# Optimization experiments

Hardware: AMD Instinct MI355X
Metric: run time of the kernel (lower is better)

## Reference

```python
import jax, jax.numpy as jnp
import numpy as np

LN_EPS = 1e-5

def setup_inputs() -> dict:
    key = jax.random.key(0)
    ks = jax.random.split(key, 8)
    B, d, var_dim, hidden = 1024, 32, 64, 256
    in_dim = d * var_dim
    causal_vars = jax.random.normal(ks[0], (B, d, var_dim), dtype=jnp.float32)
    adj_soft = jax.random.uniform(ks[1], (d, d), dtype=jnp.float32)
    # Per-variable MLP params (stacked along leading d axis), torch-default-like init scale
    s1 = 1.0 / np.sqrt(in_dim)
    s2 = 1.0 / np.sqrt(hidden)
    W1 = jax.random.uniform(ks[2], (d, in_dim, hidden), minval=-s1, maxval=s1, dtype=jnp.float32)
    b1 = jax.random.uniform(ks[3], (d, hidden), minval=-s1, maxval=s1, dtype=jnp.float32)
    W2 = jax.random.uniform(ks[4], (d, hidden, var_dim), minval=-s2, maxval=s2, dtype=jnp.float32)
    b2 = jax.random.uniform(ks[5], (d, var_dim), minval=-s2, maxval=s2, dtype=jnp.float32)
    gamma = jnp.ones((d, var_dim), dtype=jnp.float32)
    beta = jnp.zeros((d, var_dim), dtype=jnp.float32)
    return {"causal_vars": causal_vars, "adj_soft": adj_soft, "W1": W1, "b1": b1,
            "W2": W2, "b2": b2, "gamma": gamma, "beta": beta}

def reference(causal_vars, adj_soft, W1, b1, W2, b2, gamma, beta):
    B, d, var_dim = causal_vars.shape
    # masked parent input for equation i: adj_soft[i, j] * causal_vars[b, j, :]
    # shape (B, d_eq, d_parent, var_dim) -> flatten parents: (B, d, d*var_dim)
    x = adj_soft[None, :, :, None] * causal_vars[:, None, :, :]
    x = x.reshape(B, d, d * var_dim)
    # grouped 2-layer MLP, distinct weights per variable i
    h = jnp.einsum('bik,ikh->bih', x, W1) + b1[None]
    h = jax.nn.gelu(h, approximate=False)
    y = jnp.einsum('bih,ihv->biv', h, W2) + b2[None]
    # LayerNorm over var_dim with per-variable affine params
    mu = jnp.mean(y, axis=-1, keepdims=True)
    var = jnp.var(y, axis=-1, keepdims=True)
    y = (y - mu) * jax.lax.rsqrt(var + LN_EPS)
    return y * gamma[None] + beta[None]  # (B, d, var_dim)
```

## Files before the change

### kernel.cpp

```cpp
#include <hip/hip_runtime.h>
#include <hip/hip_bf16.h>

typedef __bf16 bf16_t;
typedef __bf16 bf16x8 __attribute__((ext_vector_type(8)));
typedef float f32x4 __attribute__((ext_vector_type(4)));

#define NB 1024
#define ND 32
#define VD 64
#define NH 256
#define NK 2048

#define OFF_A    0
#define OFF_W1T  (4u*1024u*1024u)
#define OFF_W2T  (36u*1024u*1024u)

#define GLD16(gsrc, ldst) \
  __builtin_amdgcn_global_load_lds((const __attribute__((address_space(1))) void*)(gsrc), \
                                   (__attribute__((address_space(3))) void*)(ldst), 16, 0, 0)

__global__ __launch_bounds__(256) void prep_kernel(
    const float* __restrict__ cv, const float* __restrict__ adj,
    const float* __restrict__ W1, const float* __restrict__ W2,
    bf16_t* __restrict__ A, bf16_t* __restrict__ W1T, bf16_t* __restrict__ W2T)
{
  __shared__ float Ls[64 * 67];
  int bx = blockIdx.x;
  int tid = threadIdx.x;
  if (bx < 4096) {
    int i = bx >> 7;
    int rem = bx & 127;
    int k0 = (rem >> 2) * 64;
    int h0 = (rem & 3) * 64;
    float a = adj[i * 32 + (k0 >> 6)];
    int rrow = tid >> 4, c4 = (tid & 15) * 4;
#pragma unroll
    for (int p = 0; p < 4; ++p) {
      int row = p * 16 + rrow;
      const float* src = W1 + ((size_t)(i * 2048 + k0 + row)) * 256 + h0 + c4;
      float4 v = *(const float4*)src;
#pragma unroll
      for (int j = 0; j < 4; ++j) Ls[row * 67 + c4 + j] = a * ((const float*)&v)[j];
    }
    __syncthreads();
#pragma unroll
    for (int p = 0; p < 2; ++p) {
      int u = p * 256 + tid;
      int h = u >> 3, c8 = u & 7;
      bf16x8 o;
#pragma unroll
      for (int j = 0; j < 8; ++j) o[j] = (bf16_t)Ls[(c8 * 8 + j) * 67 + h];
      *(bf16x8*)(W1T + ((size_t)(i * 256 + h0 + h)) * 2048 + k0 + c8 * 8) = o;
    }
  } else if (bx < 5120) {
    int t = (bx - 4096) * 256 + tid;
    const float4* s = (const float4*)cv + (size_t)t * 2;
    float4 v0 = s[0], v1 = s[1];
    bf16x8 o;
    o[0] = (bf16_t)v0.x; o[1] = (bf16_t)v0.y; o[2] = (bf16_t)v0.z; o[3] = (bf16_t)v0.w;
    o[4] = (bf16_t)v1.x; o[5] = (bf16_t)v1.y; o[6] = (bf16_t)v1.z; o[7] = (bf16_t)v1.w;
    *(bf16x8*)(A + (size_t)t * 8) = o;
  } else {
    int t = (bx - 5120) * 256 + tid;
    int i = t >> 11;
    int rem = t & 2047;
    int h8 = rem >> 6;
    int v = rem & 63;
    const float* src = W2 + ((size_t)(i * 256 + h8 * 8)) * 64 + v;
    bf16x8 o;
#pragma unroll
    for (int r = 0; r < 8; ++r) o[r] = (bf16_t)src[(size_t)r * 64];
    *(bf16x8*)(W2T + ((size_t)(i * 64 + v)) * 256 + h8 * 8) = o;
  }
}

__global__ __launch_bounds__(512, 4) void sem_main_kernel(
    const bf16_t* __restrict__ A, const bf16_t* __restrict__ W1T,
    const bf16_t* __restrict__ W2T,
    const float* __restrict__ b1, const float* __restrict__ b2,
    const float* __restrict__ gamma, const float* __restrict__ beta,
    float* __restrict__ out)
{
  __shared__ char smem[61440];

  int p = blockIdx.x;
  int L = (p & 7) * 64 + (p >> 3);
  int i = L >> 4;
  int brow = (L & 15) * 64;

  int tid = threadIdx.x;
  int lane = tid & 63;
  int wid = tid >> 6;
  int wr = wid >> 2;
  int wc = wid & 3;
  int lhi = lane >> 4;
  int llo = lane & 15;

  const bf16_t* W1Ti = W1T + (size_t)i * 256 * 2048;

  int arow = tid >> 2, ac = tid & 3;
  int sc0 = ac ^ ((arow >> 1) & 3);
  const bf16_t* aSrc  = A + (size_t)(brow + arow) * 2048 + sc0 * 8;
  const bf16_t* bSrc0 = W1Ti + (size_t)arow * 2048 + sc0 * 8;
  const bf16_t* bSrc1 = W1Ti + (size_t)(128 + arow) * 2048 + sc0 * 8;
  int ldsW = wid * 1024;

  auto stage = [&](int b, int kt) {
    char* base = smem + b * 20480;
    if (wid < 4) GLD16(aSrc + (size_t)kt * 32, base + ldsW);
    GLD16(bSrc0 + (size_t)kt * 32, base + 4096 + ldsW);
    GLD16(bSrc1 + (size_t)kt * 32, base + 12288 + ldsW);
  };

  int aOff[2], bOff[4];
#pragma unroll
  for (int m = 0; m < 2; ++m) {
    int row = wr * 32 + m * 16 + llo;
    aOff[m] = row * 64 + ((lhi ^ ((row >> 1) & 3)) * 16);
  }
#pragma unroll
  for (int n = 0; n < 4; ++n) {
    int row = wc * 64 + n * 16 + llo;
    bOff[n] = 4096 + row * 64 + ((lhi ^ ((row >> 1) & 3)) * 16);
  }

  f32x4 acc[2][4];
#pragma unroll
  for (int m = 0; m < 2; ++m)
#pragma unroll
    for (int n = 0; n < 4; ++n) acc[m][n] = (f32x4){0.f, 0.f, 0.f, 0.f};

  auto compute = [&](int b) {
    const char* base = smem + b * 20480;
    bf16x8 af[2], bfr[4];
#pragma unroll
    for (int m = 0; m < 2; ++m) af[m] = *(const bf16x8*)(base + aOff[m]);
#pragma unroll
    for (int n = 0; n < 4; ++n) bfr[n] = *(const bf16x8*)(base + bOff[n]);
    __builtin_amdgcn_s_setprio(1);
#pragma unroll
    for (int m = 0; m < 2; ++m)
#pragma unroll
      for (int n = 0; n < 4; ++n)
        acc[m][n] = __builtin_amdgcn_mfma_f32_16x16x32_bf16(af[m], bfr[n], acc[m][n], 0, 0, 0);
    __builtin_amdgcn_s_setprio(0);
  };

#define WAIT_OWN_TILE() do { \
    if (wid < 4) asm volatile("s_waitcnt vmcnt(3) lgkmcnt(0)" ::: "memory"); \
    else         asm volatile("s_waitcnt vmcnt(2) lgkmcnt(0)" ::: "memory"); \
  } while (0)

  asm volatile("" ::: "memory");
  stage(0, 0); stage(1, 1);
  int bc = 0, bs = 2;
  for (int t = 0; t < 62; ++t) {
    WAIT_OWN_TILE();
    __builtin_amdgcn_s_barrier();
    asm volatile("" ::: "memory");
    stage(bs, t + 2);
    compute(bc);
    bc = (bc == 2) ? 0 : bc + 1;
    bs = (bs == 2) ? 0 : bs + 1;
  }
  WAIT_OWN_TILE();
  __builtin_amdgcn_s_barrier();
  asm volatile("" ::: "memory");
  compute(2);
  asm volatile("s_waitcnt vmcnt(0) lgkmcnt(0)" ::: "memory");
  __builtin_amdgcn_s_barrier();
  asm volatile("" ::: "memory");
  compute(0);
  __syncthreads();

  bf16_t* Hs = (bf16_t*)smem;
  float bias[4];
#pragma unroll
  for (int n = 0; n < 4; ++n) bias[n] = b1[i * 256 + wc * 64 + n * 16 + llo];
#pragma unroll
  for (int m = 0; m < 2; ++m) {
#pragma unroll
    for (int n = 0; n < 4; ++n) {
      int col = wc * 64 + n * 16 + llo;
#pragma unroll
      for (int r = 0; r < 4; ++r) {
        int row = wr * 32 + m * 16 + lhi * 4 + r;
        float x = acc[m][n][r] + bias[n];
        float gl = 0.5f * x * (1.0f + erff(x * 0.70710678118654752f));
        Hs[row * 264 + col] = (bf16_t)gl;
      }
    }
  }
  __syncthreads();

  if (wid < 4) {
    f32x4 acc2[4];
#pragma unroll
    for (int n = 0; n < 4; ++n) acc2[n] = (f32x4){0.f, 0.f, 0.f, 0.f};
    const bf16_t* W2Ti = W2T + (size_t)i * 64 * 256;
#pragma unroll
    for (int kk = 0; kk < 8; ++kk) {
      int k = kk * 32 + lhi * 8;
      bf16x8 af = *(const bf16x8*)(Hs + (wid * 16 + llo) * 264 + k);
#pragma unroll
      for (int n = 0; n < 4; ++n) {
        bf16x8 bfr = *(const bf16x8*)(W2Ti + (size_t)(n * 16 + llo) * 256 + k);
        acc2[n] = __builtin_amdgcn_mfma_f32_16x16x32_bf16(af, bfr, acc2[n], 0, 0, 0);
      }
    }
    float b2v[4], gam[4], bet[4];
#pragma unroll
    for (int n = 0; n < 4; ++n) {
      int v = n * 16 + llo;
      b2v[n] = b2[i * 64 + v];
      gam[n] = gamma[i * 64 + v];
      bet[n] = beta[i * 64 + v];
    }
#pragma unroll
    for (int r = 0; r < 4; ++r) {
      float yv[4], s = 0.f, sq = 0.f;
#pragma unroll
      for (int n = 0; n < 4; ++n) {
        yv[n] = acc2[n][r] + b2v[n];
        s += yv[n];
        sq += yv[n] * yv[n];
      }
#pragma unroll
      for (int off = 1; off < 16; off <<= 1) {
        s += __shfl_xor(s, off, 64);
        sq += __shfl_xor(sq, off, 64);
      }
      float mu = s * (1.0f / 64.0f);
      float var = sq * (1.0f / 64.0f) - mu * mu;
      float rstd = rsqrtf(var + 1e-5f);
      int row = brow + wid * 16 + lhi * 4 + r;
      float* op = out + ((size_t)row * 32 + i) * 64;
#pragma unroll
      for (int n = 0; n < 4; ++n)
        op[n * 16 + llo] = (yv[n] - mu) * rstd * gam[n] + bet[n];
    }
  }
}

extern "C" void kernel_launch(void* const* d_in, const int* in_sizes, int n_in,
                              void* d_out, int out_size, void* d_ws, size_t ws_size,
                              hipStream_t stream) {
  const float* cv    = (const float*)d_in[0];
  const float* adj   = (const float*)d_in[1];
  const float* W1    = (const float*)d_in[2];
  const float* b1    = (const float*)d_in[3];
  const float* W2    = (const float*)d_in[4];
  const float* b2    = (const float*)d_in[5];
  const float* gamma = (const float*)d_in[6];
  const float* beta  = (const float*)d_in[7];
  float* out = (float*)d_out;

  bf16_t* Abf  = (bf16_t*)((char*)d_ws + OFF_A);
  bf16_t* W1T  = (bf16_t*)((char*)d_ws + OFF_W1T);
  bf16_t* W2T  = (bf16_t*)((char*)d_ws + OFF_W2T);

  prep_kernel<<<5376, 256, 0, stream>>>(cv, adj, W1, W2, Abf, W1T, W2T);
  sem_main_kernel<<<512, 512, 0, stream>>>(Abf, W1T, W2T, b1, b2, gamma, beta, out);
}
```

Measured before the change: 78.50 us.

## Replace LDS triple-buffered GEMM1 pipeline with direct global-to-register MFMA loads

Drops the global_load_lds triple-buffered staging, the swizzled LDS layout and the barriers in the first GEMM. Each wave now loads its MFMA fragments straight from global memory into registers in a 4x-unrolled loop, and the LDS allocation shrinks to what the hidden-activation buffer needs. This removes barrier and LDS traffic and may raise occupancy. In exchange, A and W1T tiles are no longer shared across waves, so each wave re-reads them from global or L2, and latency hiding now depends on the compiler's scheduling of the unrolled loads.

```diff
diff --git a/kernel.cpp b/kernel.cpp
--- a/kernel.cpp
+++ b/kernel.cpp
@@ -15,9 +15,7 @@
 #define OFF_W1T  (4u*1024u*1024u)
 #define OFF_W2T  (36u*1024u*1024u)
 
-#define GLD16(gsrc, ldst) \
-  __builtin_amdgcn_global_load_lds((const __attribute__((address_space(1))) void*)(gsrc), \
-                                   (__attribute__((address_space(3))) void*)(ldst), 16, 0, 0)
+#define MFMA16(AF, BF, ACC) __builtin_amdgcn_mfma_f32_16x16x32_bf16(AF, BF, ACC, 0, 0, 0)
 
 __global__ __launch_bounds__(256) void prep_kernel(
     const float* __restrict__ cv, const float* __restrict__ adj,
@@ -81,7 +79,7 @@
     const float* __restrict__ gamma, const float* __restrict__ beta,
     float* __restrict__ out)
 {
-  __shared__ char smem[61440];
+  __shared__ char smem[33792];
 
   int p = blockIdx.x;
   int L = (p & 7) * 64 + (p >> 3);
@@ -98,31 +96,8 @@
 
   const bf16_t* W1Ti = W1T + (size_t)i * 256 * 2048;
 
-  int arow = tid >> 2, ac = tid & 3;
-  int sc0 = ac ^ ((arow >> 1) & 3);
-  const bf16_t* aSrc  = A + (size_t)(brow + arow) * 2048 + sc0 * 8;
-  const bf16_t* bSrc0 = W1Ti + (size_t)arow * 2048 + sc0 * 8;
-  const bf16_t* bSrc1 = W1Ti + (size_t)(128 + arow) * 2048 + sc0 * 8;
-  int ldsW = wid * 1024;
-
-  auto stage = [&](int b, int kt) {
-    char* base = smem + b * 20480;
-    if (wid < 4) GLD16(aSrc + (size_t)kt * 32, base + ldsW);
-    GLD16(bSrc0 + (size_t)kt * 32, base + 4096 + ldsW);
-    GLD16(bSrc1 + (size_t)kt * 32, base + 12288 + ldsW);
-  };
-
-  int aOff[2], bOff[4];
-#pragma unroll
-  for (int m = 0; m < 2; ++m) {
-    int row = wr * 32 + m * 16 + llo;
-    aOff[m] = row * 64 + ((lhi ^ ((row >> 1) & 3)) * 16);
-  }
-#pragma unroll
-  for (int n = 0; n < 4; ++n) {
-    int row = wc * 64 + n * 16 + llo;
-    bOff[n] = 4096 + row * 64 + ((lhi ^ ((row >> 1) & 3)) * 16);
-  }
+  const bf16_t* aP = A + (size_t)(brow + wr * 32 + llo) * 2048 + lhi * 8;
+  const bf16_t* bP = W1Ti + (size_t)(wc * 64 + llo) * 2048 + lhi * 8;
 
   f32x4 acc[2][4];
 #pragma unroll
@@ -130,48 +105,25 @@
 #pragma unroll
     for (int n = 0; n < 4; ++n) acc[m][n] = (f32x4){0.f, 0.f, 0.f, 0.f};
 
-  auto compute = [&](int b) {
-    const char* base = smem + b * 20480;
-    bf16x8 af[2], bfr[4];
-#pragma unroll
-    for (int m = 0; m < 2; ++m) af[m] = *(const bf16x8*)(base + aOff[m]);
-#pragma unroll
-    for (int n = 0; n < 4; ++n) bfr[n] = *(const bf16x8*)(base + bOff[n]);
-    __builtin_amdgcn_s_setprio(1);
-#pragma unroll
-    for (int m = 0; m < 2; ++m)
-#pragma unroll
-      for (int n = 0; n < 4; ++n)
-        acc[m][n] = __builtin_amdgcn_mfma_f32_16x16x32_bf16(af[m], bfr[n], acc[m][n], 0, 0, 0);
-    __builtin_amdgcn_s_setprio(0);
-  };
-
-#define WAIT_OWN_TILE() do { \
-    if (wid < 4) asm volatile("s_waitcnt vmcnt(3) lgkmcnt(0)" ::: "memory"); \
-    else         asm volatile("s_waitcnt vmcnt(2) lgkmcnt(0)" ::: "memory"); \
-  } while (0)
-
-  asm volatile("" ::: "memory");
-  stage(0, 0); stage(1, 1);
-  int bc = 0, bs = 2;
-  for (int t = 0; t < 62; ++t) {
-    WAIT_OWN_TILE();
-    __builtin_amdgcn_s_barrier();
-    asm volatile("" ::: "memory");
-    stage(bs, t + 2);
-    compute(bc);
-    bc = (bc == 2) ? 0 : bc + 1;
-    bs = (bs == 2) ? 0 : bs + 1;
-  }
-  WAIT_OWN_TILE();
-  __builtin_amdgcn_s_barrier();
-  asm volatile("" ::: "memory");
-  compute(2);
-  asm volatile("s_waitcnt vmcnt(0) lgkmcnt(0)" ::: "memory");
-  __builtin_amdgcn_s_barrier();
-  asm volatile("" ::: "memory");
-  compute(0);
-  __syncthreads();
+#pragma unroll 4
+  for (int kt = 0; kt < 64; ++kt) {
+    const bf16_t* ak = aP + kt * 32;
+    const bf16_t* bk = bP + kt * 32;
+    bf16x8 af0 = *(const bf16x8*)(ak);
+    bf16x8 af1 = *(const bf16x8*)(ak + 16 * 2048);
+    bf16x8 bf0 = *(const bf16x8*)(bk);
+    bf16x8 bf1 = *(const bf16x8*)(bk + 16 * 2048);
+    bf16x8 bf2 = *(const bf16x8*)(bk + 32 * 2048);
+    bf16x8 bf3 = *(const bf16x8*)(bk + 48 * 2048);
+    acc[0][0] = MFMA16(af0, bf0, acc[0][0]);
+    acc[0][1] = MFMA16(af0, bf1, acc[0][1]);
+    acc[0][2] = MFMA16(af0, bf2, acc[0][2]);
+    acc[0][3] = MFMA16(af0, bf3, acc[0][3]);
+    acc[1][0] = MFMA16(af1, bf0, acc[1][0]);
+    acc[1][1] = MFMA16(af1, bf1, acc[1][1]);
+    acc[1][2] = MFMA16(af1, bf2, acc[1][2]);
+    acc[1][3] = MFMA16(af1, bf3, acc[1][3]);
+  }
 
   bf16_t* Hs = (bf16_t*)smem;
   float bias[4];
@@ -205,7 +157,7 @@
 #pragma unroll
       for (int n = 0; n < 4; ++n) {
         bf16x8 bfr = *(const bf16x8*)(W2Ti + (size_t)(n * 16 + llo) * 256 + k);
-        acc2[n] = __builtin_amdgcn_mfma_f32_16x16x32_bf16(af, bfr, acc2[n], 0, 0, 0);
+        acc2[n] = MFMA16(af, bfr, acc2[n]);
       }
     }
     float b2v[4], gam[4], bet[4];
```

New measurement: 202.0 us. +157.3%, slower.
